# Performance work log

Hardware: AMD Instinct MI355X
Metric: run time of the kernel (lower is better)

## Reference

```python
import jax, jax.numpy as jnp
import numpy as np

B_BASE = 512   # queries
F_IN = 16      # incoming beam width
F_OUT = 16     # outgoing beam width (cfg.B)
D = 128        # vector dim
DH = 256       # MLP hidden dim
KCB = 4096     # codebook size
A = 32         # n_codes: approximate top-k shortlist
M = 2          # previous code steps
L = 2          # residual blocks


def setup_inputs() -> dict:
    key = jax.random.key(0)
    ks = jax.random.split(key, 16)
    s = 0.05
    return {
        "x_BD": jax.random.normal(ks[0], (B_BASE, D), jnp.float32),
        "xhat_BFD": jax.random.normal(ks[1], (B_BASE, F_IN, D), jnp.float32),
        "codes_MBF": jax.random.randint(ks[2], (M, B_BASE, F_IN), 0, KCB),
        "codebook": jax.random.normal(ks[3], (KCB, D), jnp.float32) * s,
        "codebook_rq": jax.random.normal(ks[4], (KCB, D), jnp.float32) * s,
        "in_w": jax.random.normal(ks[5], (D, DH), jnp.float32) * s,
        "in_b": jnp.zeros((DH,), jnp.float32),
        "cc_w": jax.random.normal(ks[6], (DH + D, DH), jnp.float32) * s,
        "cc_b": jnp.zeros((DH,), jnp.float32),
        "rb_w1": jax.random.normal(ks[7], (L, DH, DH), jnp.float32) * s,
        "rb_b1": jnp.zeros((L, DH), jnp.float32),
        "rb_w2": jax.random.normal(ks[8], (L, DH, DH), jnp.float32) * s,
        "rb_b2": jnp.zeros((L, DH), jnp.float32),
        "out_w": jax.random.normal(ks[9], (DH, D), jnp.float32) * s,
        "out_b": jnp.zeros((D,), jnp.float32),
    }


def reference(x_BD, xhat_BFD, codes_MBF, codebook, codebook_rq,
              in_w, in_b, cc_w, cc_b, rb_w1, rb_b1, rb_w2, rb_b2,
              out_w, out_b):
    B_base, F, Dd = xhat_BFD.shape
    B = B_base * F
    xhat_BD = xhat_BFD.reshape(B, Dd)

    # --- stage 1: approximate pairwise distance (drops ||x||^2 term) + shortlist topk ---
    xt_BD = (x_BD[:, None, :] - xhat_BFD).reshape(B, Dd)           # residual targets
    cb_sq = jnp.sum(codebook_rq * codebook_rq, axis=-1)             # [K]
    dists_BK = cb_sq[None, :] - 2.0 * (xt_BD @ codebook_rq.T)       # [B, K]
    _, top_codes_BA = jax.lax.top_k(-dists_BK, A)                   # smallest-A -> [B, A]

    # --- stage 2: gather codewords, run small residual MLP on candidates ---
    cw_in = codebook[top_codes_BA].reshape(B_base, F, A, Dd)        # [Bb,F,A,D]
    h = cw_in @ in_w + in_b                                         # in_proj -> [Bb,F,A,DH]
    xb = jnp.broadcast_to(xhat_BFD[:, :, None, :], (B_base, F, A, Dd))
    h = jnp.concatenate([h, xb], axis=-1) @ cc_w + cc_b             # concat block
    for i in range(rb_w1.shape[0]):
        h = h + jax.nn.relu(h @ rb_w1[i] + rb_b1[i]) @ rb_w2[i] + rb_b2[i]
    cw = h @ out_w + out_b + cw_in                                   # out_proj + residual codeword

    # --- stage 3: exact-ish distance over beam*A candidates + beam topk ---
    cw = cw.reshape(B, A, Dd) + xhat_BD[:, None, :]                  # candidate reconstructions
    cw_flat = cw.reshape(B_base, F * A, Dd)
    d2 = jnp.sum(cw_flat * cw_flat, axis=-1) - 2.0 * jnp.einsum('bd,bkd->bk', x_BD, cw_flat)
    _, idx_BF = jax.lax.top_k(-d2, F_OUT)                            # [Bb, F_OUT]

    # --- stage 4: regather codes and reconstructions for surviving beams ---
    codes_g_BF = jnp.take_along_axis(top_codes_BA.reshape(B_base, F * A), idx_BF, axis=-1)
    codes_rep = jnp.repeat(codes_MBF, A, axis=-1)                    # [M,Bb,F*A]
    idx_M = jnp.broadcast_to(idx_BF[None], (codes_MBF.shape[0], B_base, F_OUT))
    codes_sel = jnp.take_along_axis(codes_rep, idx_M, axis=-1)       # [M,Bb,F_OUT]
    xhat_next = jnp.take_along_axis(cw_flat, idx_BF[:, :, None], axis=1)  # [Bb,F_OUT,D]
    codes_out = jnp.concatenate([codes_sel, codes_g_BF[None]], axis=0)    # [M+1,Bb,F_OUT]
    return xhat_next, codes_out
```

## Files before the change

kernel.cpp:

```cpp
#include <hip/hip_runtime.h>
#include <float.h>

typedef unsigned int u32;
typedef unsigned long long u64;
typedef unsigned short u16;
typedef __attribute__((ext_vector_type(8))) short s16x8;
typedef __attribute__((ext_vector_type(4))) float f32x4;


static __device__ __forceinline__ u32 ordu(float f) {
  u32 u = __float_as_uint(f);
  return u ^ (u32)(((int)u >> 31) | (int)0x80000000);
}
static __device__ __forceinline__ u16 f2bf(float f) {
  u32 b = __float_as_uint(f);
  b += 0x7fffu + ((b >> 16) & 1u);
  return (u16)(b >> 16);
}


__global__ __launch_bounds__(256) void k_cbrqT(const float* __restrict__ cbrq,
                                               float* __restrict__ cbT) {
  __shared__ float tile[128 * 33];
  const int k0 = blockIdx.x * 32;
  const int t = threadIdx.x;
#pragma unroll
  for (int rep = 0; rep < 16; ++rep) {
    const int flat = rep * 256 + t;
    const int kk = flat >> 7, d = flat & 127;
    tile[d * 33 + kk] = cbrq[(k0 + kk) * 128 + d];
  }
  __syncthreads();
#pragma unroll
  for (int rep = 0; rep < 16; ++rep) {
    const int flat = rep * 256 + t;
    const int d = flat >> 5, kk = flat & 31;
    cbT[d * 4096 + k0 + kk] = tile[d * 33 + kk];
  }
}

__global__ __launch_bounds__(256) void k_cbsq(const float* __restrict__ cbT,
                                              float* __restrict__ cb_sq) {
  const int k = blockIdx.x * 256 + threadIdx.x;
  float r[8];
#pragma unroll
  for (int j = 0; j < 8; ++j) {
    const float v = cbT[j * 4096 + k];
    r[j] = __fmul_rn(v, v);
  }
  for (int i = 8; i < 128; i += 8) {
#pragma unroll
    for (int j = 0; j < 8; ++j) {
      const float v = cbT[(i + j) * 4096 + k];
      r[j] = __fadd_rn(r[j], __fmul_rn(v, v));
    }
  }
  cb_sq[k] = __fadd_rn(
      __fadd_rn(__fadd_rn(r[0], r[1]), __fadd_rn(r[2], r[3])),
      __fadd_rn(__fadd_rn(r[4], r[5]), __fadd_rn(r[6], r[7])));
}

__global__ __launch_bounds__(256) void k_xt(const float* __restrict__ x,
                                            const float* __restrict__ xhat,
                                            float* __restrict__ xt) {
  const int i = blockIdx.x * 256 + threadIdx.x;
  const int row = i >> 5, d4 = i & 31;
  const float4 a = ((const float4*)x)[(row >> 4) * 32 + d4];
  const float4 b = ((const float4*)xhat)[i];
  float4 r;
  r.x = __fsub_rn(a.x, b.x); r.y = __fsub_rn(a.y, b.y);
  r.z = __fsub_rn(a.z, b.z); r.w = __fsub_rn(a.w, b.w);
  ((float4*)xt)[i] = r;
}

__global__ __launch_bounds__(256) void k_codeh(const float* __restrict__ cb,
                                               const float* __restrict__ in_w,
                                               const float* __restrict__ in_b,
                                               float* __restrict__ tmp_h) {
  __shared__ float row[128];
  const int code = blockIdx.x;
  const int t = threadIdx.x;
  if (t < 128) row[t] = cb[code * 128 + t];
  __syncthreads();
  float a = 0.f;
  for (int d = 0; d < 128; ++d) a = __builtin_fmaf(row[d], in_w[d * 256 + t], a);
  tmp_h[code * 256 + t] = __fadd_rn(a, in_b[t]);
}

__global__ __launch_bounds__(256) void k_biasprep(
    const float* __restrict__ rb_b1, const float* __restrict__ rb_b2,
    const float* __restrict__ rb_w1, const float* __restrict__ out_w,
    const float* __restrict__ out_b, float* __restrict__ bias2v,
    float* __restrict__ biasDv) {
  const int t = threadIdx.x;
  const float* w11 = rb_w1 + 65536;
  float s = rb_b1[256 + t];
  for (int i = 0; i < 256; ++i) s += rb_b2[i] * w11[i * 256 + t];
  bias2v[t] = s;
  if (t < 128) {
    float s2 = out_b[t];
    for (int i = 0; i < 256; ++i)
      s2 += (rb_b2[i] + rb_b2[256 + i]) * out_w[i * 128 + t];
    biasDv[t] = s2;
  }
}

__global__ __launch_bounds__(256) void k_wfrag(
    const float* __restrict__ W21, const float* __restrict__ V1,
    const float* __restrict__ V2, u16* __restrict__ W21f,
    u16* __restrict__ V1f, u16* __restrict__ V2f) {
  const int gid = blockIdx.x * 256 + threadIdx.x;
  const int l = gid & 63;
  const int grp = gid >> 6;
  const int kq = (l >> 4) * 8;
  const int nn = l & 15;
  if (grp < 128) {
    const int kt = grp >> 4, nt = grp & 15;
    u16* dst = W21f + (size_t)(grp * 64 + l) * 8;
#pragma unroll
    for (int j = 0; j < 8; ++j)
      dst[j] = f2bf(W21[(kt * 32 + kq + j) * 256 + nt * 16 + nn]);
  } else if (grp < 192) {
    const int g2 = grp - 128, kt = g2 >> 3, nt = g2 & 7;
    u16* dst = V1f + (size_t)(g2 * 64 + l) * 8;
#pragma unroll
    for (int j = 0; j < 8; ++j)
      dst[j] = f2bf(V1[(kt * 32 + kq + j) * 128 + nt * 16 + nn]);
  } else {
    const int g2 = grp - 192, kt = g2 >> 3, nt = g2 & 7;
    u16* dst = V2f + (size_t)(g2 * 64 + l) * 8;
#pragma unroll
    for (int j = 0; j < 8; ++j)
      dst[j] = f2bf(V2[(kt * 32 + kq + j) * 128 + nt * 16 + nn]);
  }
}

__global__ __launch_bounds__(256, 4) void gemm_f32(
    const float* __restrict__ Am, const float* __restrict__ Bm,
    float* __restrict__ Cm, const int Mi, const int Ni, const int Ki,
    const float* __restrict__ bias, const float* __restrict__ addm) {
  __shared__ float As[16][68];
  __shared__ float Bs[16][68];
  const int m0 = blockIdx.x * 64, n0 = blockIdx.y * 64;
  const int t = threadIdx.x;
  const int tm = (t & 15) * 4, tn = (t >> 4) * 4;
  float acc[4][4] = {};
  for (int k0 = 0; k0 < Ki; k0 += 16) {
    {
      const int row = t >> 2, q = t & 3;
      const float4 a4 = *(const float4*)(Am + (size_t)(m0 + row) * Ki + k0 + q * 4);
      As[q * 4 + 0][row] = a4.x; As[q * 4 + 1][row] = a4.y;
      As[q * 4 + 2][row] = a4.z; As[q * 4 + 3][row] = a4.w;
      const int kk = t >> 4, n4 = t & 15;
      *(float4*)&Bs[kk][n4 * 4] =
          *(const float4*)(Bm + (size_t)(k0 + kk) * Ni + n0 + n4 * 4);
    }
    __syncthreads();
#pragma unroll
    for (int kk = 0; kk < 16; ++kk) {
      const float4 av = *(const float4*)&As[kk][tm];
      const float4 bv = *(const float4*)&Bs[kk][tn];
      const float aa[4] = {av.x, av.y, av.z, av.w};
      const float bb[4] = {bv.x, bv.y, bv.z, bv.w};
#pragma unroll
      for (int i = 0; i < 4; ++i)
#pragma unroll
        for (int j = 0; j < 4; ++j) acc[i][j] += aa[i] * bb[j];
    }
    __syncthreads();
  }
#pragma unroll
  for (int i = 0; i < 4; ++i) {
    const int m = m0 + tm + i;
#pragma unroll
    for (int j = 0; j < 4; ++j) {
      const int n = n0 + tn + j;
      float v = acc[i][j];
      if (bias) v += bias[n];
      if (addm) v += addm[(size_t)m * Ni + n];
      Cm[(size_t)m * Ni + n] = v;
    }
  }
}

__global__ __launch_bounds__(512, 2) void k_stage1(
    const float* __restrict__ xt, const float* __restrict__ cbT,
    const float* __restrict__ cb_sq, int* __restrict__ topc) {
  __shared__ u32 distL[4 * 4096];
  __shared__ float xtL[512];
  const int r0 = blockIdx.x * 4;
  const int t = threadIdx.x;
  xtL[t] = xt[r0 * 128 + t];
  __syncthreads();
  {
    const int k0 = t * 8;
    float acc[4][8] = {};
    for (int d = 0; d < 128; ++d) {
      const float4 c0 = *(const float4*)&cbT[d * 4096 + k0];
      const float4 c1 = *(const float4*)&cbT[d * 4096 + k0 + 4];
      const float cv[8] = {c0.x, c0.y, c0.z, c0.w, c1.x, c1.y, c1.z, c1.w};
      const float x0 = xtL[d], x1 = xtL[128 + d], x2 = xtL[256 + d],
                  x3 = xtL[384 + d];
#pragma unroll
      for (int j = 0; j < 8; ++j) {
        acc[0][j] = __builtin_fmaf(x0, cv[j], acc[0][j]);
        acc[1][j] = __builtin_fmaf(x1, cv[j], acc[1][j]);
        acc[2][j] = __builtin_fmaf(x2, cv[j], acc[2][j]);
        acc[3][j] = __builtin_fmaf(x3, cv[j], acc[3][j]);
      }
    }
    const float4 s0 = *(const float4*)&cb_sq[k0];
    const float4 s1 = *(const float4*)&cb_sq[k0 + 4];
    const float cs[8] = {s0.x, s0.y, s0.z, s0.w, s1.x, s1.y, s1.z, s1.w};
#pragma unroll
    for (int rr = 0; rr < 4; ++rr)
#pragma unroll
      for (int j = 0; j < 8; ++j)
        distL[rr * 4096 + k0 + j] =
            ordu(__fsub_rn(cs[j], __fmul_rn(2.0f, acc[rr][j])));
  }
  __syncthreads();
  const int w = t >> 6, lane = t & 63;
  if (w < 4) {
    u32* dr = distL + w * 4096;
    u64 m1 = ~0ull, m2 = ~0ull;
    for (int e = 0; e < 64; ++e) {
      const int idx = e * 64 + lane;
      const u64 key = ((u64)dr[idx] << 32) | (u32)idx;
      if (key < m1) { m2 = m1; m1 = key; } else if (key < m2) { m2 = key; }
    }
    bool have2 = true;
    for (int it = 0; it < 32; ++it) {
      u64 g = m1;
#pragma unroll
      for (int sh = 1; sh < 64; sh <<= 1) {
        const u64 o = __shfl_xor(g, sh);
        g = (o < g) ? o : g;
      }
      const int bi = (int)(g & 0xFFFFFFFFu);
      if (lane == 0) topc[(r0 + w) * 32 + it] = bi;
      if ((bi & 63) == lane) {
        dr[bi] = 0xFFFFFFFFu;
        if (have2) {
          m1 = m2; m2 = ~0ull; have2 = false;
        } else {
          m1 = m2 = ~0ull;
          for (int e = 0; e < 64; ++e) {
            const int idx = e * 64 + lane;
            const u64 key = ((u64)dr[idx] << 32) | (u32)idx;
            if (key < m1) { m2 = m1; m1 = key; } else if (key < m2) { m2 = key; }
          }
          have2 = true;
        }
      }
    }
  }
}

__global__ __launch_bounds__(256, 4) void k_mlp(
    const int* __restrict__ topc, const float* __restrict__ A1,
    const float* __restrict__ A2, const float* __restrict__ B1,
    const float* __restrict__ B2, const float* __restrict__ Dc,
    const float* __restrict__ Dr, const u16* __restrict__ W21f,
    const u16* __restrict__ V1f, const u16* __restrict__ V2f,
    const float* __restrict__ xhat, const float* __restrict__ x,
    float* __restrict__ d2g) {
  __shared__ __align__(16) u16 abuf[32 * 264];
  __shared__ float B1r[256];
  __shared__ int codesL[32];
  __shared__ float d2red[32][4];

  const int tt = threadIdx.x;
  const int br = blockIdx.x;
  const int bb = br >> 4;
  const int w = tt >> 6, l = tt & 63;

  B1r[tt] = B1[br * 256 + tt];
  if (tt < 32) codesL[tt] = topc[br * 32 + tt];
  __syncthreads();

  {
    const int c = tt & 31, g = tt >> 5;
    const int code = codesL[c];
    const float4* A14 = (const float4*)(A1 + code * 256 + g * 32);
    u32* dst = (u32*)(abuf + c * 264 + g * 32);
#pragma unroll
    for (int e4 = 0; e4 < 8; ++e4) {
      const float4 a = A14[e4];
      const int i = g * 32 + e4 * 4;
      const u32 p0 = (u32)f2bf(fmaxf(a.x + B1r[i], 0.f)) |
                     ((u32)f2bf(fmaxf(a.y + B1r[i + 1], 0.f)) << 16);
      const u32 p1 = (u32)f2bf(fmaxf(a.z + B1r[i + 2], 0.f)) |
                     ((u32)f2bf(fmaxf(a.w + B1r[i + 3], 0.f)) << 16);
      dst[e4 * 2] = p0;
      dst[e4 * 2 + 1] = p1;
    }
  }
  __syncthreads();

  const int arow = l & 15;
  const int kq = (l >> 4) * 8;
  const s16x8* wf = (const s16x8*)W21f;
  const s16x8* v1f = (const s16x8*)V1f;
  const s16x8* v2f = (const s16x8*)V2f;
  const f32x4 zero4 = {0.f, 0.f, 0.f, 0.f};

  f32x4 accf[2][4];
#pragma unroll
  for (int mt = 0; mt < 2; ++mt)
#pragma unroll
    for (int ntl = 0; ntl < 4; ++ntl) accf[mt][ntl] = zero4;
  for (int kt = 0; kt < 8; ++kt) {
    const s16x8 a0 = *(const s16x8*)(abuf + arow * 264 + kt * 32 + kq);
    const s16x8 a1 = *(const s16x8*)(abuf + (16 + arow) * 264 + kt * 32 + kq);
#pragma unroll
    for (int ntl = 0; ntl < 4; ++ntl) {
      const s16x8 b = wf[(kt * 16 + w * 4 + ntl) * 64 + l];
      accf[0][ntl] =
          __builtin_amdgcn_mfma_f32_16x16x32_bf16(a0, b, accf[0][ntl], 0, 0, 0);
      accf[1][ntl] =
          __builtin_amdgcn_mfma_f32_16x16x32_bf16(a1, b, accf[1][ntl], 0, 0, 0);
    }
  }

  f32x4 acc2f[2][2];
#pragma unroll
  for (int mt = 0; mt < 2; ++mt)
#pragma unroll
    for (int ntl = 0; ntl < 2; ++ntl) acc2f[mt][ntl] = zero4;
  for (int kt = 0; kt < 8; ++kt) {
    const s16x8 a0 = *(const s16x8*)(abuf + arow * 264 + kt * 32 + kq);
    const s16x8 a1 = *(const s16x8*)(abuf + (16 + arow) * 264 + kt * 32 + kq);
#pragma unroll
    for (int ntl = 0; ntl < 2; ++ntl) {
      const s16x8 b = v1f[(kt * 8 + w * 2 + ntl) * 64 + l];
      acc2f[0][ntl] = __builtin_amdgcn_mfma_f32_16x16x32_bf16(
          a0, b, acc2f[0][ntl], 0, 0, 0);
      acc2f[1][ntl] = __builtin_amdgcn_mfma_f32_16x16x32_bf16(
          a1, b, acc2f[1][ntl], 0, 0, 0);
    }
  }

  u16 r2v[2][4][4];
#pragma unroll
  for (int mt = 0; mt < 2; ++mt)
#pragma unroll
    for (int ntl = 0; ntl < 4; ++ntl) {
      const int n = w * 64 + ntl * 16 + arow;
      const float b2 = B2[br * 256 + n];
      const f32x4 cf = accf[mt][ntl];
#pragma unroll
      for (int rg = 0; rg < 4; ++rg) {
        const int m = mt * 16 + (l >> 4) * 4 + rg;
        const float a2 = A2[codesL[m] * 256 + n];
        r2v[mt][ntl][rg] = f2bf(fmaxf(cf[rg] + a2 + b2, 0.f));
      }
    }
  __syncthreads();
#pragma unroll
  for (int mt = 0; mt < 2; ++mt)
#pragma unroll
    for (int ntl = 0; ntl < 4; ++ntl) {
      const int n = w * 64 + ntl * 16 + arow;
#pragma unroll
      for (int rg = 0; rg < 4; ++rg) {
        const int m = mt * 16 + (l >> 4) * 4 + rg;
        abuf[m * 264 + n] = r2v[mt][ntl][rg];
      }
    }
  __syncthreads();

  for (int kt = 0; kt < 8; ++kt) {
    const s16x8 a0 = *(const s16x8*)(abuf + arow * 264 + kt * 32 + kq);
    const s16x8 a1 = *(const s16x8*)(abuf + (16 + arow) * 264 + kt * 32 + kq);
#pragma unroll
    for (int ntl = 0; ntl < 2; ++ntl) {
      const s16x8 b = v2f[(kt * 8 + w * 2 + ntl) * 64 + l];
      acc2f[0][ntl] = __builtin_amdgcn_mfma_f32_16x16x32_bf16(
          a0, b, acc2f[0][ntl], 0, 0, 0);
      acc2f[1][ntl] = __builtin_amdgcn_mfma_f32_16x16x32_bf16(
          a1, b, acc2f[1][ntl], 0, 0, 0);
    }
  }

  float sm[2][4];
#pragma unroll
  for (int mt = 0; mt < 2; ++mt)
#pragma unroll
    for (int rg = 0; rg < 4; ++rg) sm[mt][rg] = 0.f;
#pragma unroll
  for (int ntl = 0; ntl < 2; ++ntl) {
    const int d = w * 32 + ntl * 16 + arow;
    const float dr = Dr[br * 128 + d];
    const float xh = xhat[br * 128 + d];
    const float xq = x[bb * 128 + d];
#pragma unroll
    for (int mt = 0; mt < 2; ++mt) {
      const f32x4 cf = acc2f[mt][ntl];
#pragma unroll
      for (int rg = 0; rg < 4; ++rg) {
        const int m = mt * 16 + (l >> 4) * 4 + rg;
        const float cand = cf[rg] + Dc[codesL[m] * 128 + d] + dr + xh;
        sm[mt][rg] += cand * cand - 2.f * xq * cand;
      }
    }
  }
#pragma unroll
  for (int mt = 0; mt < 2; ++mt)
#pragma unroll
    for (int rg = 0; rg < 4; ++rg) {
      float s = sm[mt][rg];
      s += __shfl_xor(s, 1);
      s += __shfl_xor(s, 2);
      s += __shfl_xor(s, 4);
      s += __shfl_xor(s, 8);
      if (arow == 0) d2red[mt * 16 + (l >> 4) * 4 + rg][w] = s;
    }
  __syncthreads();
  if (tt < 32)
    d2g[bb * 512 + (br & 15) * 32 + tt] =
        d2red[tt][0] + d2red[tt][1] + d2red[tt][2] + d2red[tt][3];
}

__global__ __launch_bounds__(64, 1) void k_sel32(const float* __restrict__ d2g,
                                                 int* __restrict__ sel32) {
  __shared__ u32 d2u[512];
  const int bb = blockIdx.x;
  const int t = threadIdx.x;
  for (int i = t; i < 512; i += 64) d2u[i] = ordu(d2g[bb * 512 + i]);
  __syncthreads();
  for (int it = 0; it < 32; ++it) {
    u64 m = ~0ull;
#pragma unroll
    for (int e = 0; e < 8; ++e) {
      const int idx = e * 64 + t;
      const u64 key = ((u64)d2u[idx] << 32) | (u32)idx;
      m = (key < m) ? key : m;
    }
#pragma unroll
    for (int sh = 1; sh < 64; sh <<= 1) {
      const u64 o = __shfl_xor(m, sh);
      m = (o < m) ? o : m;
    }
    const int s = (int)(m & 0xFFFFFFFFu);
    if ((s & 63) == t) d2u[s] = 0xFFFFFFFFu;
    if (t == 0) sel32[bb * 32 + it] = s;
  }
}

__global__ __launch_bounds__(256, 4) void k_rescore(
    const int* __restrict__ sel32, const int* __restrict__ topc,
    const float* __restrict__ tmp_h, const float* __restrict__ cb,
    const float* __restrict__ xhat, const float* __restrict__ x,
    const float* __restrict__ cc_w, const float* __restrict__ cc_b,
    const float* __restrict__ rb_w1, const float* __restrict__ rb_b1,
    const float* __restrict__ rb_w2, const float* __restrict__ rb_b2,
    const float* __restrict__ out_w, const float* __restrict__ out_b,
    float* __restrict__ d2r, float* __restrict__ candv) {
  __shared__ float A_[8][256], B_[8][256], C_[8][256];
  __shared__ float cbL[8][128], xhL[8][128], candL[8][128], xqL[128];
  __shared__ int codeL[8], rowL[8];
  const int bb = blockIdx.x >> 2;
  const int j0 = (blockIdx.x & 3) * 8;
  const int t = threadIdx.x;
  if (t < 8) {
    const int s = sel32[bb * 32 + j0 + t];
    rowL[t] = bb * 16 + (s >> 5);
    codeL[t] = topc[(bb * 16 + (s >> 5)) * 32 + (s & 31)];
  }
  if (t < 128) xqL[t] = x[bb * 128 + t];
  __syncthreads();
  for (int idx = t; idx < 1024; idx += 256) {
    const int c = idx >> 7, d = idx & 127;
    cbL[c][d] = cb[codeL[c] * 128 + d];
    xhL[c][d] = xhat[rowL[c] * 128 + d];
  }
  for (int idx = t; idx < 2048; idx += 256) {
    const int c = idx >> 8, i = idx & 255;
    A_[c][i] = tmp_h[codeL[c] * 256 + i];
  }
  __syncthreads();
  {
    float acc[8] = {};
    for (int i = 0; i < 256; i += 4) {
      const float w0 = cc_w[(i + 0) * 256 + t], w1 = cc_w[(i + 1) * 256 + t];
      const float w2 = cc_w[(i + 2) * 256 + t], w3 = cc_w[(i + 3) * 256 + t];
#pragma unroll
      for (int c = 0; c < 8; ++c) {
        const float4 h = *(const float4*)&A_[c][i];
        acc[c] = __builtin_fmaf(h.x, w0, acc[c]);
        acc[c] = __builtin_fmaf(h.y, w1, acc[c]);
        acc[c] = __builtin_fmaf(h.z, w2, acc[c]);
        acc[c] = __builtin_fmaf(h.w, w3, acc[c]);
      }
    }
    for (int d = 0; d < 128; d += 4) {
      const float w0 = cc_w[(256 + d + 0) * 256 + t];
      const float w1 = cc_w[(256 + d + 1) * 256 + t];
      const float w2 = cc_w[(256 + d + 2) * 256 + t];
      const float w3 = cc_w[(256 + d + 3) * 256 + t];
#pragma unroll
      for (int c = 0; c < 8; ++c) {
        const float4 h = *(const float4*)&xhL[c][d];
        acc[c] = __builtin_fmaf(h.x, w0, acc[c]);
        acc[c] = __builtin_fmaf(h.y, w1, acc[c]);
        acc[c] = __builtin_fmaf(h.z, w2, acc[c]);
        acc[c] = __builtin_fmaf(h.w, w3, acc[c]);
      }
    }
    const float b = cc_b[t];
#pragma unroll
    for (int c = 0; c < 8; ++c) B_[c][t] = __fadd_rn(acc[c], b);
  }
  __syncthreads();
  {
    float acc[8] = {};
    for (int i = 0; i < 256; i += 4) {
      const float w0 = rb_w1[(i + 0) * 256 + t], w1 = rb_w1[(i + 1) * 256 + t];
      const float w2 = rb_w1[(i + 2) * 256 + t], w3 = rb_w1[(i + 3) * 256 + t];
#pragma unroll
      for (int c = 0; c < 8; ++c) {
        const float4 h = *(const float4*)&B_[c][i];
        acc[c] = __builtin_fmaf(h.x, w0, acc[c]);
        acc[c] = __builtin_fmaf(h.y, w1, acc[c]);
        acc[c] = __builtin_fmaf(h.z, w2, acc[c]);
        acc[c] = __builtin_fmaf(h.w, w3, acc[c]);
      }
    }
    const float b = rb_b1[t];
#pragma unroll
    for (int c = 0; c < 8; ++c) C_[c][t] = fmaxf(__fadd_rn(acc[c], b), 0.f);
  }
  __syncthreads();
  {
    float acc[8] = {};
    for (int i = 0; i < 256; i += 4) {
      const float w0 = rb_w2[(i + 0) * 256 + t], w1 = rb_w2[(i + 1) * 256 + t];
      const float w2 = rb_w2[(i + 2) * 256 + t], w3 = rb_w2[(i + 3) * 256 + t];
#pragma unroll
      for (int c = 0; c < 8; ++c) {
        const float4 h = *(const float4*)&C_[c][i];
        acc[c] = __builtin_fmaf(h.x, w0, acc[c]);
        acc[c] = __builtin_fmaf(h.y, w1, acc[c]);
        acc[c] = __builtin_fmaf(h.z, w2, acc[c]);
        acc[c] = __builtin_fmaf(h.w, w3, acc[c]);
      }
    }
    const float b = rb_b2[t];
#pragma unroll
    for (int c = 0; c < 8; ++c)
      A_[c][t] = __fadd_rn(__fadd_rn(B_[c][t], acc[c]), b);
  }
  __syncthreads();
  {
    float acc[8] = {};
    const float* w11 = rb_w1 + 65536;
    for (int i = 0; i < 256; i += 4) {
      const float w0 = w11[(i + 0) * 256 + t], w1 = w11[(i + 1) * 256 + t];
      const float w2 = w11[(i + 2) * 256 + t], w3 = w11[(i + 3) * 256 + t];
#pragma unroll
      for (int c = 0; c < 8; ++c) {
        const float4 h = *(const float4*)&A_[c][i];
        acc[c] = __builtin_fmaf(h.x, w0, acc[c]);
        acc[c] = __builtin_fmaf(h.y, w1, acc[c]);
        acc[c] = __builtin_fmaf(h.z, w2, acc[c]);
        acc[c] = __builtin_fmaf(h.w, w3, acc[c]);
      }
    }
    const float b = rb_b1[256 + t];
#pragma unroll
    for (int c = 0; c < 8; ++c) B_[c][t] = fmaxf(__fadd_rn(acc[c], b), 0.f);
  }
  __syncthreads();
  {
    float acc[8] = {};
    const float* w21 = rb_w2 + 65536;
    for (int i = 0; i < 256; i += 4) {
      const float w0 = w21[(i + 0) * 256 + t], w1 = w21[(i + 1) * 256 + t];
      const float w2 = w21[(i + 2) * 256 + t], w3 = w21[(i + 3) * 256 + t];
#pragma unroll
      for (int c = 0; c < 8; ++c) {
        const float4 h = *(const float4*)&B_[c][i];
        acc[c] = __builtin_fmaf(h.x, w0, acc[c]);
        acc[c] = __builtin_fmaf(h.y, w1, acc[c]);
        acc[c] = __builtin_fmaf(h.z, w2, acc[c]);
        acc[c] = __builtin_fmaf(h.w, w3, acc[c]);
      }
    }
    const float b = rb_b2[256 + t];
#pragma unroll
    for (int c = 0; c < 8; ++c)
      C_[c][t] = __fadd_rn(__fadd_rn(A_[c][t], acc[c]), b);
  }
  __syncthreads();
  if (t < 128) {
    float acc[8] = {};
    for (int i = 0; i < 256; i += 4) {
      const float w0 = out_w[(i + 0) * 128 + t], w1 = out_w[(i + 1) * 128 + t];
      const float w2 = out_w[(i + 2) * 128 + t], w3 = out_w[(i + 3) * 128 + t];
#pragma unroll
      for (int c = 0; c < 8; ++c) {
        const float4 h = *(const float4*)&C_[c][i];
        acc[c] = __builtin_fmaf(h.x, w0, acc[c]);
        acc[c] = __builtin_fmaf(h.y, w1, acc[c]);
        acc[c] = __builtin_fmaf(h.z, w2, acc[c]);
        acc[c] = __builtin_fmaf(h.w, w3, acc[c]);
      }
    }
    const float ob = out_b[t];
#pragma unroll
    for (int c = 0; c < 8; ++c) {
      const float cw_ = __fadd_rn(__fadd_rn(acc[c], ob), cbL[c][t]);
      const float cand = __fadd_rn(cw_, xhL[c][t]);
      candL[c][t] = cand;
      candv[(bb * 32 + j0 + c) * 128 + t] = cand;
    }
  }
  __syncthreads();
  if (t < 8) {
    float r[8];
#pragma unroll
    for (int j = 0; j < 8; ++j) {
      const float v = candL[t][j];
      r[j] = __fmul_rn(v, v);
    }
    for (int i = 8; i < 128; i += 8) {
#pragma unroll
      for (int j = 0; j < 8; ++j) {
        const float v = candL[t][i + j];
        r[j] = __fadd_rn(r[j], __fmul_rn(v, v));
      }
    }
    const float s1f = __fadd_rn(
        __fadd_rn(__fadd_rn(r[0], r[1]), __fadd_rn(r[2], r[3])),
        __fadd_rn(__fadd_rn(r[4], r[5]), __fadd_rn(r[6], r[7])));
    double s2 = 0.0;
    for (int d = 0; d < 128; ++d)
      s2 += (double)xqL[d] * (double)candL[t][d];
    const float s2f = (float)s2;
    d2r[bb * 32 + j0 + t] = __fsub_rn(s1f, __fmul_rn(2.0f, s2f));
  }
}

__global__ __launch_bounds__(64, 1) void k_final(
    const float* __restrict__ d2r, const int* __restrict__ sel32,
    const int* __restrict__ topc, const int* __restrict__ codes_in,
    const float* __restrict__ candv, float* __restrict__ out) {
  __shared__ u32 winLo[16];
  const int bb = blockIdx.x;
  const int t = threadIdx.x;
  u64 key = ~0ull;
  if (t < 32) {
    const u32 s = (u32)sel32[bb * 32 + t];
    key = ((u64)ordu(d2r[bb * 32 + t]) << 32) | (s << 5) | (u32)t;
  }
  for (int it = 0; it < 16; ++it) {
    u64 m = key;
#pragma unroll
    for (int sh = 1; sh < 64; sh <<= 1) {
      const u64 o = __shfl_xor(m, sh);
      m = (o < m) ? o : m;
    }
    if (key == m) key = ~0ull;
    if (t == 0) winLo[it] = (u32)(m & 0xFFFFFFFFu);
  }
  __syncthreads();
  if (t < 16) {
    const u32 lo = winLo[t];
    const int s = (int)((lo >> 5) & 511u);
    const int f = s >> 5;
    const int code = topc[(bb * 16 + f) * 32 + (s & 31)];
    float* oc = out + 512 * 16 * 128;
    oc[bb * 16 + t] = (float)codes_in[bb * 16 + f];
    oc[8192 + bb * 16 + t] = (float)codes_in[8192 + bb * 16 + f];
    oc[16384 + bb * 16 + t] = (float)code;
  }
  __syncthreads();
  for (int idx = t; idx < 2048; idx += 64) {
    const int w_ = idx >> 7, d = idx & 127;
    const int j = (int)(winLo[w_] & 31u);
    out[(bb * 16 + w_) * 128 + d] = candv[(bb * 32 + j) * 128 + d];
  }
}

extern "C" void kernel_launch(void* const* d_in, const int* in_sizes, int n_in,
                              void* d_out, int out_size, void* d_ws,
                              size_t ws_size, hipStream_t stream) {
  const float* x = (const float*)d_in[0];
  const float* xhat = (const float*)d_in[1];
  const int* codes = (const int*)d_in[2];
  const float* cb = (const float*)d_in[3];
  const float* cbrq = (const float*)d_in[4];
  const float* in_w = (const float*)d_in[5];
  const float* in_b = (const float*)d_in[6];
  const float* cc_w = (const float*)d_in[7];
  const float* cc_b = (const float*)d_in[8];
  const float* rb_w1 = (const float*)d_in[9];
  const float* rb_b1 = (const float*)d_in[10];
  const float* rb_w2 = (const float*)d_in[11];
  const float* rb_b2 = (const float*)d_in[12];
  const float* out_w = (const float*)d_in[13];
  const float* out_b = (const float*)d_in[14];
  float* out = (float*)d_out;

  float* ws = (float*)d_ws;
  size_t o = 0;
  float* cb_sq = ws + o; o += 4096;
  float* xt = ws + o;    const size_t xt_off = o; o += (size_t)8192 * 128;
  float* cbT = ws + o;   o += (size_t)128 * 4096;
  float* tmp_h = ws + o; o += (size_t)4096 * 256;
  float* pc = ws + o;    const size_t pc_off = o; o += (size_t)4096 * 256;
  float* pb = ws + o;    o += (size_t)8192 * 256;
  float* A1 = ws + o;    o += (size_t)4096 * 256;
  float* A2 = ws + o;    o += (size_t)4096 * 256;
  float* Dc = ws + o;    o += (size_t)4096 * 128;
  float* B1 = ws + o;    o += (size_t)8192 * 256;
  float* B2 = ws + o;    o += (size_t)8192 * 256;
  float* Dr = ws + o;    o += (size_t)8192 * 128;
  float* W21 = ws + o;   o += 65536;
  float* V1 = ws + o;    o += 32768;
  float* V2 = ws + o;    o += 32768;
  float* bias2v = ws + o; o += 256;
  float* biasDv = ws + o; o += 128;
  int* topc = (int*)(ws + o); o += 262144;
  float* d2g = ws + o;   o += 262144;
  u16* W21f = (u16*)(ws + o); o += 32768;
  u16* V1f = (u16*)(ws + o);  o += 16384;
  u16* V2f = (u16*)(ws + o);  o += 16384;
  float* d2r = ws + xt_off;
  int* sel32 = (int*)(ws + xt_off + 16384);
  float* candv = ws + pc_off;

  k_cbrqT<<<dim3(128), dim3(256), 0, stream>>>(cbrq, cbT);
  k_cbsq<<<dim3(16), dim3(256), 0, stream>>>(cbT, cb_sq);
  k_xt<<<dim3(1024), dim3(256), 0, stream>>>(x, xhat, xt);
  k_biasprep<<<dim3(1), dim3(256), 0, stream>>>(rb_b1, rb_b2, rb_w1, out_w,
                                                out_b, bias2v, biasDv);
  k_codeh<<<dim3(4096), dim3(256), 0, stream>>>(cb, in_w, in_b, tmp_h);
  gemm_f32<<<dim3(64, 4), dim3(256), 0, stream>>>(tmp_h, cc_w, pc, 4096, 256,
                                                  256, nullptr, nullptr);
  gemm_f32<<<dim3(128, 4), dim3(256), 0, stream>>>(xhat, cc_w + 256 * 256, pb,
                                                   8192, 256, 128, cc_b,
                                                   nullptr);
  gemm_f32<<<dim3(64, 4), dim3(256), 0, stream>>>(pc, rb_w1, A1, 4096, 256, 256,
                                                  nullptr, nullptr);
  gemm_f32<<<dim3(64, 4), dim3(256), 0, stream>>>(pc, rb_w1 + 65536, A2, 4096,
                                                  256, 256, nullptr, nullptr);
  gemm_f32<<<dim3(64, 2), dim3(256), 0, stream>>>(pc, out_w, Dc, 4096, 128, 256,
                                                  nullptr, cb);
  gemm_f32<<<dim3(128, 4), dim3(256), 0, stream>>>(pb, rb_w1, B1, 8192, 256,
                                                   256, rb_b1, nullptr);
  gemm_f32<<<dim3(128, 4), dim3(256), 0, stream>>>(pb, rb_w1 + 65536, B2, 8192,
                                                   256, 256, bias2v, nullptr);
  gemm_f32<<<dim3(128, 2), dim3(256), 0, stream>>>(pb, out_w, Dr, 8192, 128,
                                                   256, biasDv, nullptr);
  gemm_f32<<<dim3(4, 4), dim3(256), 0, stream>>>(rb_w2, rb_w1 + 65536, W21, 256,
                                                 256, 256, nullptr, nullptr);
  gemm_f32<<<dim3(4, 2), dim3(256), 0, stream>>>(rb_w2, out_w, V1, 256, 128,
                                                 256, nullptr, nullptr);
  gemm_f32<<<dim3(4, 2), dim3(256), 0, stream>>>(rb_w2 + 65536, out_w, V2, 256,
                                                 128, 256, nullptr, nullptr);
  k_wfrag<<<dim3(64), dim3(256), 0, stream>>>(W21, V1, V2, W21f, V1f, V2f);

  k_stage1<<<dim3(2048), dim3(512), 0, stream>>>(xt, cbT, cb_sq, topc);
  k_mlp<<<dim3(8192), dim3(256), 0, stream>>>(topc, A1, A2, B1, B2, Dc, Dr,
                                              W21f, V1f, V2f, xhat, x, d2g);
  k_sel32<<<dim3(512), dim3(64), 0, stream>>>(d2g, sel32);
  k_rescore<<<dim3(2048), dim3(256), 0, stream>>>(
      sel32, topc, tmp_h, cb, xhat, x, cc_w, cc_b, rb_w1, rb_b1, rb_w2, rb_b2,
      out_w, out_b, d2r, candv);
  k_final<<<dim3(512), dim3(64), 0, stream>>>(d2r, sel32, topc, codes, candv,
                                              out);
  (void)in_sizes; (void)n_in; (void)out_size; (void)ws_size;
}
```

Before: 910.3 us.

## Fold cc_w into downstream weights to skip intermediate projections

Precomposes cc_w with the concatenated rb_w1/out_w weights (Wcat) so the code-side and beam-side precompute becomes one fused GEMM each, with scattered outputs and folded bias vectors. This drops the pc/pb intermediate GEMMs and their memory traffic and cuts the number of kernel launches. In k_rescore it removes the cbL and candL shared buffers, reusing B_ and reading cb directly, and raises the occupancy hint to 5 blocks. Reassociating the fp32 products changes rounding slightly, and candv moves to its own workspace region.

```diff
diff --git a/kernel.cpp b/kernel.cpp
--- a/kernel.cpp
+++ b/kernel.cpp
@@ -87,21 +87,40 @@
   tmp_h[code * 256 + t] = __fadd_rn(a, in_b[t]);
 }
 
+__global__ __launch_bounds__(256) void k_pack(const float* __restrict__ rb_w1,
+                                              const float* __restrict__ out_w,
+                                              float* __restrict__ Wcat) {
+  const int i = blockIdx.x;
+  const int t = threadIdx.x;
+  Wcat[i * 640 + t] = rb_w1[i * 256 + t];
+  Wcat[i * 640 + 256 + t] = rb_w1[65536 + i * 256 + t];
+  if (t < 128) Wcat[i * 640 + 512 + t] = out_w[i * 128 + t];
+}
+
 __global__ __launch_bounds__(256) void k_biasprep(
     const float* __restrict__ rb_b1, const float* __restrict__ rb_b2,
     const float* __restrict__ rb_w1, const float* __restrict__ out_w,
-    const float* __restrict__ out_b, float* __restrict__ bias2v,
-    float* __restrict__ biasDv) {
+    const float* __restrict__ out_b, const float* __restrict__ cc_b,
+    const float* __restrict__ Wcat, float* __restrict__ cvec) {
   const int t = threadIdx.x;
   const float* w11 = rb_w1 + 65536;
-  float s = rb_b1[256 + t];
-  for (int i = 0; i < 256; ++i) s += rb_b2[i] * w11[i * 256 + t];
-  bias2v[t] = s;
+  float b2v = rb_b1[256 + t];
+  for (int i = 0; i < 256; ++i) b2v += rb_b2[i] * w11[i * 256 + t];
+  float c0 = rb_b1[t], c1 = b2v;
+  for (int i = 0; i < 256; ++i) {
+    const float cbi = cc_b[i];
+    c0 += cbi * Wcat[i * 640 + t];
+    c1 += cbi * Wcat[i * 640 + 256 + t];
+  }
+  cvec[t] = c0;
+  cvec[256 + t] = c1;
   if (t < 128) {
-    float s2 = out_b[t];
+    float bDv = out_b[t];
     for (int i = 0; i < 256; ++i)
-      s2 += (rb_b2[i] + rb_b2[256 + i]) * out_w[i * 128 + t];
-    biasDv[t] = s2;
+      bDv += (rb_b2[i] + rb_b2[256 + i]) * out_w[i * 128 + t];
+    float c2 = bDv;
+    for (int i = 0; i < 256; ++i) c2 += cc_b[i] * Wcat[i * 640 + 512 + t];
+    cvec[512 + t] = c2;
   }
 }
 
@@ -179,6 +198,61 @@
       if (bias) v += bias[n];
       if (addm) v += addm[(size_t)m * Ni + n];
       Cm[(size_t)m * Ni + n] = v;
+    }
+  }
+}
+
+__global__ __launch_bounds__(256, 4) void gemm_scatter(
+    const float* __restrict__ Am, const float* __restrict__ Bm, const int Mi,
+    const int Ki, const float* __restrict__ bias,
+    const float* __restrict__ add3, float* __restrict__ O1,
+    float* __restrict__ O2, float* __restrict__ O3) {
+  __shared__ float As[16][68];
+  __shared__ float Bs[16][68];
+  const int m0 = blockIdx.x * 64, n0 = blockIdx.y * 64;
+  const int t = threadIdx.x;
+  const int tm = (t & 15) * 4, tn = (t >> 4) * 4;
+  float acc[4][4] = {};
+  for (int k0 = 0; k0 < Ki; k0 += 16) {
+    {
+      const int row = t >> 2, q = t & 3;
+      const float4 a4 = *(const float4*)(Am + (size_t)(m0 + row) * Ki + k0 + q * 4);
+      As[q * 4 + 0][row] = a4.x; As[q * 4 + 1][row] = a4.y;
+      As[q * 4 + 2][row] = a4.z; As[q * 4 + 3][row] = a4.w;
+      const int kk = t >> 4, n4 = t & 15;
+      *(float4*)&Bs[kk][n4 * 4] =
+          *(const float4*)(Bm + (size_t)(k0 + kk) * 640 + n0 + n4 * 4);
+    }
+    __syncthreads();
+#pragma unroll
+    for (int kk = 0; kk < 16; ++kk) {
+      const float4 av = *(const float4*)&As[kk][tm];
+      const float4 bv = *(const float4*)&Bs[kk][tn];
+      const float aa[4] = {av.x, av.y, av.z, av.w};
+      const float bb[4] = {bv.x, bv.y, bv.z, bv.w};
+#pragma unroll
+      for (int i = 0; i < 4; ++i)
+#pragma unroll
+        for (int j = 0; j < 4; ++j) acc[i][j] += aa[i] * bb[j];
+    }
+    __syncthreads();
+  }
+#pragma unroll
+  for (int i = 0; i < 4; ++i) {
+    const int m = m0 + tm + i;
+#pragma unroll
+    for (int j = 0; j < 4; ++j) {
+      const int n = n0 + tn + j;
+      float v = acc[i][j];
+      if (bias) v += bias[n];
+      if (n < 256) {
+        O1[(size_t)m * 256 + n] = v;
+      } else if (n < 512) {
+        O2[(size_t)m * 256 + n - 256] = v;
+      } else {
+        if (add3) v += add3[(size_t)m * 128 + n - 512];
+        O3[(size_t)m * 128 + n - 512] = v;
+      }
     }
   }
 }
@@ -448,7 +522,7 @@
   }
 }
 
-__global__ __launch_bounds__(256, 4) void k_rescore(
+__global__ __launch_bounds__(256, 5) void k_rescore(
     const int* __restrict__ sel32, const int* __restrict__ topc,
     const float* __restrict__ tmp_h, const float* __restrict__ cb,
     const float* __restrict__ xhat, const float* __restrict__ x,
@@ -458,7 +532,7 @@
     const float* __restrict__ out_w, const float* __restrict__ out_b,
     float* __restrict__ d2r, float* __restrict__ candv) {
   __shared__ float A_[8][256], B_[8][256], C_[8][256];
-  __shared__ float cbL[8][128], xhL[8][128], candL[8][128], xqL[128];
+  __shared__ float xhL[8][128], xqL[128];
   __shared__ int codeL[8], rowL[8];
   const int bb = blockIdx.x >> 2;
   const int j0 = (blockIdx.x & 3) * 8;
@@ -472,7 +546,6 @@
   __syncthreads();
   for (int idx = t; idx < 1024; idx += 256) {
     const int c = idx >> 7, d = idx & 127;
-    cbL[c][d] = cb[codeL[c] * 128 + d];
     xhL[c][d] = xhat[rowL[c] * 128 + d];
   }
   for (int idx = t; idx < 2048; idx += 256) {
@@ -610,9 +683,10 @@
     const float ob = out_b[t];
 #pragma unroll
     for (int c = 0; c < 8; ++c) {
-      const float cw_ = __fadd_rn(__fadd_rn(acc[c], ob), cbL[c][t]);
+      const float cbv = cb[codeL[c] * 128 + t];
+      const float cw_ = __fadd_rn(__fadd_rn(acc[c], ob), cbv);
       const float cand = __fadd_rn(cw_, xhL[c][t]);
-      candL[c][t] = cand;
+      B_[c][t] = cand;
       candv[(bb * 32 + j0 + c) * 128 + t] = cand;
     }
   }
@@ -621,13 +695,13 @@
     float r[8];
 #pragma unroll
     for (int j = 0; j < 8; ++j) {
-      const float v = candL[t][j];
+      const float v = B_[t][j];
       r[j] = __fmul_rn(v, v);
     }
     for (int i = 8; i < 128; i += 8) {
 #pragma unroll
       for (int j = 0; j < 8; ++j) {
-        const float v = candL[t][i + j];
+        const float v = B_[t][i + j];
         r[j] = __fadd_rn(r[j], __fmul_rn(v, v));
       }
     }
@@ -636,7 +710,7 @@
         __fadd_rn(__fadd_rn(r[4], r[5]), __fadd_rn(r[6], r[7])));
     double s2 = 0.0;
     for (int d = 0; d < 128; ++d)
-      s2 += (double)xqL[d] * (double)candL[t][d];
+      s2 += (double)xqL[d] * (double)B_[t][d];
     const float s2f = (float)s2;
     d2r[bb * 32 + j0 + t] = __fsub_rn(s1f, __fmul_rn(2.0f, s2f));
   }
@@ -709,8 +783,10 @@
   float* xt = ws + o;    const size_t xt_off = o; o += (size_t)8192 * 128;
   float* cbT = ws + o;   o += (size_t)128 * 4096;
   float* tmp_h = ws + o; o += (size_t)4096 * 256;
-  float* pc = ws + o;    const size_t pc_off = o; o += (size_t)4096 * 256;
-  float* pb = ws + o;    o += (size_t)8192 * 256;
+  float* Wcat = ws + o;  o += (size_t)256 * 640;
+  float* M_A = ws + o;   o += (size_t)256 * 640;
+  float* M_B = ws + o;   o += (size_t)128 * 640;
+  float* cvec = ws + o;  o += 640;
   float* A1 = ws + o;    o += (size_t)4096 * 256;
   float* A2 = ws + o;    o += (size_t)4096 * 256;
   float* Dc = ws + o;    o += (size_t)4096 * 128;
@@ -720,40 +796,31 @@
   float* W21 = ws + o;   o += 65536;
   float* V1 = ws + o;    o += 32768;
   float* V2 = ws + o;    o += 32768;
-  float* bias2v = ws + o; o += 256;
-  float* biasDv = ws + o; o += 128;
   int* topc = (int*)(ws + o); o += 262144;
   float* d2g = ws + o;   o += 262144;
   u16* W21f = (u16*)(ws + o); o += 32768;
   u16* V1f = (u16*)(ws + o);  o += 16384;
   u16* V2f = (u16*)(ws + o);  o += 16384;
+  float* candv = ws + o; o += (size_t)16384 * 128;
   float* d2r = ws + xt_off;
   int* sel32 = (int*)(ws + xt_off + 16384);
-  float* candv = ws + pc_off;
 
   k_cbrqT<<<dim3(128), dim3(256), 0, stream>>>(cbrq, cbT);
   k_cbsq<<<dim3(16), dim3(256), 0, stream>>>(cbT, cb_sq);
   k_xt<<<dim3(1024), dim3(256), 0, stream>>>(x, xhat, xt);
+  k_codeh<<<dim3(4096), dim3(256), 0, stream>>>(cb, in_w, in_b, tmp_h);
+  k_pack<<<dim3(256), dim3(256), 0, stream>>>(rb_w1, out_w, Wcat);
   k_biasprep<<<dim3(1), dim3(256), 0, stream>>>(rb_b1, rb_b2, rb_w1, out_w,
-                                                out_b, bias2v, biasDv);
-  k_codeh<<<dim3(4096), dim3(256), 0, stream>>>(cb, in_w, in_b, tmp_h);
-  gemm_f32<<<dim3(64, 4), dim3(256), 0, stream>>>(tmp_h, cc_w, pc, 4096, 256,
+                                                out_b, cc_b, Wcat, cvec);
+  gemm_f32<<<dim3(4, 10), dim3(256), 0, stream>>>(cc_w, Wcat, M_A, 256, 640,
                                                   256, nullptr, nullptr);
-  gemm_f32<<<dim3(128, 4), dim3(256), 0, stream>>>(xhat, cc_w + 256 * 256, pb,
-                                                   8192, 256, 128, cc_b,
-                                                   nullptr);
-  gemm_f32<<<dim3(64, 4), dim3(256), 0, stream>>>(pc, rb_w1, A1, 4096, 256, 256,
-                                                  nullptr, nullptr);
-  gemm_f32<<<dim3(64, 4), dim3(256), 0, stream>>>(pc, rb_w1 + 65536, A2, 4096,
-                                                  256, 256, nullptr, nullptr);
-  gemm_f32<<<dim3(64, 2), dim3(256), 0, stream>>>(pc, out_w, Dc, 4096, 128, 256,
-                                                  nullptr, cb);
-  gemm_f32<<<dim3(128, 4), dim3(256), 0, stream>>>(pb, rb_w1, B1, 8192, 256,
-                                                   256, rb_b1, nullptr);
-  gemm_f32<<<dim3(128, 4), dim3(256), 0, stream>>>(pb, rb_w1 + 65536, B2, 8192,
-                                                   256, 256, bias2v, nullptr);
-  gemm_f32<<<dim3(128, 2), dim3(256), 0, stream>>>(pb, out_w, Dr, 8192, 128,
-                                                   256, biasDv, nullptr);
+  gemm_f32<<<dim3(2, 10), dim3(256), 0, stream>>>(cc_w + 256 * 256, Wcat, M_B,
+                                                  128, 640, 256, nullptr,
+                                                  nullptr);
+  gemm_scatter<<<dim3(64, 10), dim3(256), 0, stream>>>(
+      tmp_h, M_A, 4096, 256, nullptr, cb, A1, A2, Dc);
+  gemm_scatter<<<dim3(128, 10), dim3(256), 0, stream>>>(
+      xhat, M_B, 8192, 128, cvec, nullptr, B1, B2, Dr);
   gemm_f32<<<dim3(4, 4), dim3(256), 0, stream>>>(rb_w2, rb_w1 + 65536, W21, 256,
                                                  256, 256, nullptr, nullptr);
   gemm_f32<<<dim3(4, 2), dim3(256), 0, stream>>>(rb_w2, out_w, V1, 256, 128,
```

New measurement: 892.0 us. -2.0%, faster.
